# Optimization experiments

Measured on AMD Instinct MI355X. Metric: run time of the kernel, lower is better.

Reference implementation:

```python
import jax, jax.numpy as jnp
import numpy as np

SLOPE = 25.0   # snntorch surrogate.fast_sigmoid default slope
THR = 1.0      # snntorch Leaky default threshold
NUM_STEPS = 100

# fast_sigmoid surrogate spike: heaviside fwd, 1/(slope|x|+1)^2 bwd
@jax.custom_vjp
def spike(x):
    return (x > 0).astype(x.dtype)

def _spike_fwd(x):
    return spike(x), x

def _spike_bwd(x, g):
    return (g / (SLOPE * jnp.abs(x) + 1.0) ** 2,)

spike.defvjp(_spike_fwd, _spike_bwd)


def setup_inputs() -> dict:
    key = jax.random.key(0)
    ks = jax.random.split(key, 5)
    B, D_in, D_h, D_out = 512, 784, 2048, 10
    x = jax.random.normal(ks[0], (B, D_in), dtype=jnp.float32)
    W1 = jax.random.normal(ks[1], (D_h, D_in), dtype=jnp.float32) / np.sqrt(D_in).astype(np.float32)
    b1 = jax.random.normal(ks[2], (D_h,), dtype=jnp.float32) * 0.01
    W2 = jax.random.normal(ks[3], (D_out, D_h), dtype=jnp.float32) / np.sqrt(D_h).astype(np.float32)
    b2 = jax.random.normal(ks[4], (D_out,), dtype=jnp.float32) * 0.01
    beta1 = jnp.asarray(0.9, dtype=jnp.float32)  # learn_beta=True -> parameter
    beta2 = jnp.asarray(0.9, dtype=jnp.float32)
    return {"x": x, "W1": W1, "b1": b1, "W2": W2, "b2": b2, "beta1": beta1, "beta2": beta2}


def reference(x, W1, b1, W2, b2, beta1, beta2):
    dtype = x.dtype
    B = x.shape[0]
    Dh = W1.shape[0]
    Do = W2.shape[0]
    # fc1(x) is loop-invariant in the original (x constant across steps) -> hoist
    cur1 = x @ W1.T + b1                       # [B, Dh]
    b1c = jnp.clip(beta1, 0.0, 1.0)            # snntorch clamps beta in forward
    b2c = jnp.clip(beta2, 0.0, 1.0)
    mem1_0 = jnp.zeros((B, Dh), dtype)         # init_leaky -> 0
    mem2_0 = jnp.zeros((B, Do), dtype)

    def step(carry, _):
        mem1, mem2 = carry
        # snntorch Leaky (reset_mechanism='subtract'):
        # reset_t = detached heaviside(mem_{t-1} - thr); mem_t = beta*mem_{t-1} + cur - reset*thr
        reset1 = jax.lax.stop_gradient((mem1 > THR).astype(dtype))
        mem1 = b1c * mem1 + cur1 - reset1 * THR
        spk1 = spike(mem1 - THR)               # [B, Dh]
        cur2 = spk1 @ W2.T + b2                # [B, Do]
        reset2 = jax.lax.stop_gradient((mem2 > THR).astype(dtype))
        mem2 = b2c * mem2 + cur2 - reset2 * THR
        spk2 = spike(mem2 - THR)
        return (mem1, mem2), spk2

    _, spk2_rec = jax.lax.scan(step, (mem1_0, mem2_0), None, length=NUM_STEPS)  # [T, B, Do]
    # snn_res_step_num == snn_num_steps -> mean over all steps
    stk_mean = jnp.mean(spk2_rec, axis=0)      # [B, Do]
    return jax.nn.softmax(stk_mean, axis=1)
```

## Files before the change

kernel.cpp:

```cpp
#include <hip/hip_runtime.h>
#include <cstdint>

typedef unsigned int u32;
typedef unsigned short u16;
typedef unsigned long long u64;
typedef __attribute__((ext_vector_type(4))) float f32x4;
typedef __attribute__((ext_vector_type(8))) short s16x8;

#define D_IN   784
#define D_H    2048
#define D_O    10
#define T_STEPS 100
#define NCOPY  16

static __device__ __forceinline__ u16 f2bf_rn(float f) {
  u32 u = __float_as_uint(f);
  u32 r = u + 0x7FFFu + ((u >> 16) & 1u);
  return (u16)(r >> 16);
}
static __device__ __forceinline__ float bf2f(u16 h) {
  return __uint_as_float(((u32)h) << 16);
}

static __device__ __forceinline__ void packpair(float f0, float f1,
                                                u32& o0, u32& o1, u32& o2) {
  u32 u0 = __float_as_uint(f0), u1 = __float_as_uint(f1);
  o0 = (u0 >> 16) | (u1 & 0xFFFF0000u);
  float r0 = __fsub_rn(f0, __uint_as_float(u0 & 0xFFFF0000u));
  float r1 = __fsub_rn(f1, __uint_as_float(u1 & 0xFFFF0000u));
  u32 v0 = __float_as_uint(r0), v1 = __float_as_uint(r1);
  o1 = (v0 >> 16) | (v1 & 0xFFFF0000u);
  float s0 = __fsub_rn(r0, __uint_as_float(v0 & 0xFFFF0000u));
  float s1 = __fsub_rn(r1, __uint_as_float(v1 & 0xFFFF0000u));
  o2 = (__float_as_uint(s0) >> 16) | (__float_as_uint(s1) & 0xFFFF0000u);
}

__global__ __launch_bounds__(256) void k_prep_w2(const float* __restrict__ W2,
                                                 u32* __restrict__ Phi,
                                                 u32* __restrict__ Plo) {
  const int blk = blockIdx.x;
  const int copy = blk >> 4;
  int t = (blk & 15) * 256 + threadIdx.x;
  int kb = t >> 6, l = t & 63;
  int o = l & 15;
  int kbase = kb * 32 + ((l >> 4) << 3);
  u32 hw[4], lw[4];
#pragma unroll
  for (int p = 0; p < 4; ++p) {
    u32 hp = 0, lp = 0;
#pragma unroll
    for (int q = 0; q < 2; ++q) {
      float f = (o < D_O) ? W2[o * D_H + kbase + 2 * p + q] : 0.0f;
      u16 h = f2bf_rn(f);
      float rr = __fsub_rn(f, bf2f(h));
      u16 lo = f2bf_rn(rr);
      hp |= ((u32)h) << (16 * q);
      lp |= ((u32)lo) << (16 * q);
    }
    hw[p] = hp; lw[p] = lp;
  }
  int base = (copy << 15) + (kb * 64 + l) * 4;
#pragma unroll
  for (int p = 0; p < 4; ++p) { Phi[base + p] = hw[p]; Plo[base + p] = lw[p]; }
}

__global__ __launch_bounds__(512) void k_fgemm(const float* __restrict__ x,
                                               const float* __restrict__ W1,
                                               const float* __restrict__ b1,
                                               float* __restrict__ cur1) {
  __shared__ uint4 As[2][3][4][64];
  __shared__ uint4 Bs[2][3][4][64];
  const int tid = threadIdx.x, wave = tid >> 6, lane = tid & 63;
  const int id = blockIdx.x;
  const int sub = id >> 3;
  const int mb = sub >> 2;
  const int nb = (id & 7) * 4 + (sub & 3);
  const int wm = wave >> 1, wn = wave & 1;
  const int st = tid & 255;
  const int srow = st >> 2, skq = st & 3;
  const int sfrag = srow >> 4;
  const int slane = skq * 16 + (srow & 15);
  const bool isA = (tid < 256);
  const float* srcrow = isA ? (x  + (size_t)(mb * 64 + srow) * D_IN)
                            : (W1 + (size_t)(nb * 64 + srow) * D_IN);
  f32x4 acc0 = {0.f, 0.f, 0.f, 0.f}, acc1 = {0.f, 0.f, 0.f, 0.f};
  float e[8];
  {
    const int kg = skq * 8;
    float4 v0 = *(const float4*)(srcrow + kg);
    float4 v1 = *(const float4*)(srcrow + kg + 4);
    e[0] = v0.x; e[1] = v0.y; e[2] = v0.z; e[3] = v0.w;
    e[4] = v1.x; e[5] = v1.y; e[6] = v1.z; e[7] = v1.w;
  }
  {
    u32 w0[4], w1[4], w2[4];
#pragma unroll
    for (int p = 0; p < 4; ++p) packpair(e[2 * p], e[2 * p + 1], w0[p], w1[p], w2[p]);
    if (isA) {
      As[0][0][sfrag][slane] = make_uint4(w0[0], w0[1], w0[2], w0[3]);
      As[0][1][sfrag][slane] = make_uint4(w1[0], w1[1], w1[2], w1[3]);
      As[0][2][sfrag][slane] = make_uint4(w2[0], w2[1], w2[2], w2[3]);
    } else {
      Bs[0][0][sfrag][slane] = make_uint4(w0[0], w0[1], w0[2], w0[3]);
      Bs[0][1][sfrag][slane] = make_uint4(w1[0], w1[1], w1[2], w1[3]);
      Bs[0][2][sfrag][slane] = make_uint4(w2[0], w2[1], w2[2], w2[3]);
    }
  }
  __syncthreads();
  for (int kb = 0; kb < 25; ++kb) {
    const int cur = kb & 1, nxt = cur ^ 1;
    if (kb < 24) {
      const int kg = (kb + 1) * 32 + skq * 8;
      if (kg < D_IN) {
        float4 v0 = *(const float4*)(srcrow + kg);
        float4 v1 = *(const float4*)(srcrow + kg + 4);
        e[0] = v0.x; e[1] = v0.y; e[2] = v0.z; e[3] = v0.w;
        e[4] = v1.x; e[5] = v1.y; e[6] = v1.z; e[7] = v1.w;
      } else {
#pragma unroll
        for (int q = 0; q < 8; ++q) e[q] = 0.0f;
      }
    }
    s16x8 A0 = __builtin_bit_cast(s16x8, As[cur][0][wm][lane]);
    s16x8 A1 = __builtin_bit_cast(s16x8, As[cur][1][wm][lane]);
    s16x8 A2 = __builtin_bit_cast(s16x8, As[cur][2][wm][lane]);
    {
      s16x8 B0 = __builtin_bit_cast(s16x8, Bs[cur][0][wn * 2][lane]);
      s16x8 B1 = __builtin_bit_cast(s16x8, Bs[cur][1][wn * 2][lane]);
      s16x8 B2 = __builtin_bit_cast(s16x8, Bs[cur][2][wn * 2][lane]);
      acc0 = __builtin_amdgcn_mfma_f32_16x16x32_bf16(A0, B0, acc0, 0, 0, 0);
      acc0 = __builtin_amdgcn_mfma_f32_16x16x32_bf16(A0, B1, acc0, 0, 0, 0);
      acc0 = __builtin_amdgcn_mfma_f32_16x16x32_bf16(A1, B0, acc0, 0, 0, 0);
      acc0 = __builtin_amdgcn_mfma_f32_16x16x32_bf16(A1, B1, acc0, 0, 0, 0);
      acc0 = __builtin_amdgcn_mfma_f32_16x16x32_bf16(A0, B2, acc0, 0, 0, 0);
      acc0 = __builtin_amdgcn_mfma_f32_16x16x32_bf16(A2, B0, acc0, 0, 0, 0);
    }
    {
      s16x8 B0 = __builtin_bit_cast(s16x8, Bs[cur][0][wn * 2 + 1][lane]);
      s16x8 B1 = __builtin_bit_cast(s16x8, Bs[cur][1][wn * 2 + 1][lane]);
      s16x8 B2 = __builtin_bit_cast(s16x8, Bs[cur][2][wn * 2 + 1][lane]);
      acc1 = __builtin_amdgcn_mfma_f32_16x16x32_bf16(A0, B0, acc1, 0, 0, 0);
      acc1 = __builtin_amdgcn_mfma_f32_16x16x32_bf16(A0, B1, acc1, 0, 0, 0);
      acc1 = __builtin_amdgcn_mfma_f32_16x16x32_bf16(A1, B0, acc1, 0, 0, 0);
      acc1 = __builtin_amdgcn_mfma_f32_16x16x32_bf16(A1, B1, acc1, 0, 0, 0);
      acc1 = __builtin_amdgcn_mfma_f32_16x16x32_bf16(A0, B2, acc1, 0, 0, 0);
      acc1 = __builtin_amdgcn_mfma_f32_16x16x32_bf16(A2, B0, acc1, 0, 0, 0);
    }
    if (kb < 24) {
      u32 w0[4], w1[4], w2[4];
#pragma unroll
      for (int p = 0; p < 4; ++p) packpair(e[2 * p], e[2 * p + 1], w0[p], w1[p], w2[p]);
      if (isA) {
        As[nxt][0][sfrag][slane] = make_uint4(w0[0], w0[1], w0[2], w0[3]);
        As[nxt][1][sfrag][slane] = make_uint4(w1[0], w1[1], w1[2], w1[3]);
        As[nxt][2][sfrag][slane] = make_uint4(w2[0], w2[1], w2[2], w2[3]);
      } else {
        Bs[nxt][0][sfrag][slane] = make_uint4(w0[0], w0[1], w0[2], w0[3]);
        Bs[nxt][1][sfrag][slane] = make_uint4(w1[0], w1[1], w1[2], w1[3]);
        Bs[nxt][2][sfrag][slane] = make_uint4(w2[0], w2[1], w2[2], w2[3]);
      }
    }
    __syncthreads();
  }
  const int col = lane & 15, rb = (lane >> 4) * 4;
  {
    const int gcol = nb * 64 + (wn * 2) * 16 + col;
    const float bv = b1[gcol];
#pragma unroll
    for (int r = 0; r < 4; ++r)
      cur1[(size_t)(mb * 64 + wm * 16 + rb + r) * D_H + gcol] = acc0[r] + bv;
  }
  {
    const int gcol = nb * 64 + (wn * 2 + 1) * 16 + col;
    const float bv = b1[gcol];
#pragma unroll
    for (int r = 0; r < 4; ++r)
      cur1[(size_t)(mb * 64 + wm * 16 + rb + r) * D_H + gcol] = acc1[r] + bv;
  }
}

__global__ __launch_bounds__(512) void k_snn4(const float* __restrict__ cur1,
                                              const u32* __restrict__ Phi,
                                              const u32* __restrict__ Plo,
                                              const float* __restrict__ b2,
                                              const float* __restrict__ beta1p,
                                              const float* __restrict__ beta2p,
                                              float* __restrict__ out) {
  __shared__ __align__(16) u32 bits[112][66];
  __shared__ float c2[112][18];
  const int b = blockIdx.x;
  const int tid = threadIdx.x;
  const int wave = tid >> 6, lane = tid & 63;
  const float b1c = fminf(fmaxf(beta1p[0], 0.0f), 1.0f);
  const float b2c = fminf(fmaxf(beta2p[0], 0.0f), 1.0f);

  for (int idx = tid; idx < 12 * 66; idx += 512) bits[100 + idx / 66][idx % 66] = 0;

  float cv[4], memv[4], spf[4];
#pragma unroll
  for (int j = 0; j < 4; ++j) {
    cv[j] = cur1[(size_t)b * D_H + j * 512 + tid];
    memv[j] = 0.0f; spf[j] = 0.0f;
  }
  for (int t = 0; t < T_STEPS; ++t) {
    u64 msk[4];
#pragma unroll
    for (int j = 0; j < 4; ++j) {
      float m = __fmul_rn(b1c, memv[j]);
      m = __fadd_rn(m, cv[j]);
      m = __fsub_rn(m, spf[j]);
      bool sp = (m > 1.0f);
      msk[j] = __ballot(sp);
      spf[j] = sp ? 1.0f : 0.0f;
      memv[j] = m;
    }
    if (lane == 0) {
      u64* rowp = (u64*)&bits[t][0];
      rowp[0 * 8 + wave] = msk[0];
      rowp[1 * 8 + wave] = msk[1];
      rowp[2 * 8 + wave] = msk[2];
      rowp[3 * 8 + wave] = msk[3];
    }
  }
  __syncthreads();

  if (wave < 7) {
    const u32* PhiB = Phi + ((size_t)(b & (NCOPY - 1)) << 15);
    const u32* PloB = Plo + ((size_t)(b & (NCOPY - 1)) << 15);
    f32x4 acc = {0.f, 0.f, 0.f, 0.f};
    const int row0 = wave * 16 + (lane & 15);
    const int shift = (lane >> 4) * 8;
    for (int kg = 0; kg < 64; kg += 4) {
      uint4 bh[4], bl[4];
#pragma unroll
      for (int i = 0; i < 4; ++i) {
        bh[i] = *(const uint4*)(PhiB + (size_t)(kg + i) * 256 + lane * 4);
        bl[i] = *(const uint4*)(PloB + (size_t)(kg + i) * 256 + lane * 4);
      }
#pragma unroll
      for (int i = 0; i < 4; ++i) {
        u32 w8 = (bits[row0][kg + i] >> shift) & 0xFFu;
        u32 u = w8 | (w8 << 15);
        uint4 a0u;
        ((u32*)&a0u)[0] = ( u        & 0x00010001u) * 0x3F80u;
        ((u32*)&a0u)[1] = ((u >> 2)  & 0x00010001u) * 0x3F80u;
        ((u32*)&a0u)[2] = ((u >> 4)  & 0x00010001u) * 0x3F80u;
        ((u32*)&a0u)[3] = ((u >> 6)  & 0x00010001u) * 0x3F80u;
        s16x8 a   = __builtin_bit_cast(s16x8, a0u);
        s16x8 bhi = __builtin_bit_cast(s16x8, bh[i]);
        s16x8 blo = __builtin_bit_cast(s16x8, bl[i]);
        acc = __builtin_amdgcn_mfma_f32_16x16x32_bf16(a, bhi, acc, 0, 0, 0);
        acc = __builtin_amdgcn_mfma_f32_16x16x32_bf16(a, blo, acc, 0, 0, 0);
      }
    }
    const int colw = lane & 15, rbase = (lane >> 4) * 4;
#pragma unroll
    for (int r = 0; r < 4; ++r) c2[wave * 16 + rbase + r][colw] = acc[r];
  }
  __syncthreads();

  if (tid < 16) {
    const int o = tid;
    const bool valid = (o < D_O);
    const float bb = valid ? b2[o] : 0.0f;
    float m2 = 0.0f; bool s2 = false; int cnt = 0;
    for (int t0 = 0; t0 < T_STEPS; t0 += 10) {
      float cc[10];
#pragma unroll
      for (int i = 0; i < 10; ++i) cc[i] = c2[t0 + i][o];
#pragma unroll
      for (int i = 0; i < 10; ++i) {
        float cI = __fadd_rn(cc[i], bb);
        float m = __fadd_rn(__fmul_rn(b2c, m2), cI);
        if (s2) m = __fsub_rn(m, 1.0f);
        s2 = (m > 1.0f);
        m2 = m;
        cnt += s2 ? 1 : 0;
      }
    }
    float mean = valid ? ((float)cnt / 100.0f) : -1e30f;
    float mx = mean;
#pragma unroll
    for (int i = 8; i >= 1; i >>= 1) mx = fmaxf(mx, __shfl_xor(mx, i, 16));
    float e = valid ? expf(mean - mx) : 0.0f;
    float s = e;
#pragma unroll
    for (int i = 8; i >= 1; i >>= 1) s = __fadd_rn(s, __shfl_xor(s, i, 16));
    if (valid) out[(size_t)b * D_O + o] = e / s;
  }
}

extern "C" void kernel_launch(void* const* d_in, const int* in_sizes, int n_in,
                              void* d_out, int out_size, void* d_ws, size_t ws_size,
                              hipStream_t stream) {
  const float* x     = (const float*)d_in[0];
  const float* W1    = (const float*)d_in[1];
  const float* b1    = (const float*)d_in[2];
  const float* W2    = (const float*)d_in[3];
  const float* b2    = (const float*)d_in[4];
  const float* beta1 = (const float*)d_in[5];
  const float* beta2 = (const float*)d_in[6];
  float* out = (float*)d_out;

  char* ws = (char*)d_ws;
  float* cur1 = (float*)ws;
  u32*   Phi  = (u32*)(ws + 4194304);
  u32*   Plo  = (u32*)(ws + 6291456);

  hipLaunchKernelGGL(k_prep_w2, dim3(256), dim3(256), 0, stream, W2, Phi, Plo);
  hipLaunchKernelGGL(k_fgemm, dim3(256), dim3(512), 0, stream, x, W1, b1, cur1);
  hipLaunchKernelGGL(k_snn4, dim3(512), dim3(512), 0, stream,
                     cur1, Phi, Plo, b2, beta1, beta2, out);
}
```

Baseline: 67.26 us.

## Stage W2 fragments through LDS with async double-buffered loads, drop W2 copies

The spike-by-W2 GEMM in the SNN kernel now streams W2 bf16 hi/lo fragments into shared memory using global_load_lds in a double-buffered loop. All eight waves cooperatively load each chunk while seven waves run MFMAs. This replaces per-wave direct global loads from 16 replicated W2 copies, so the prep kernel shrinks to one copy and 16 blocks. Launch-bounds occupancy hints are also added to the GEMM and SNN kernels. The cost is extra __syncthreads per chunk and about 32KB more LDS per block, which may limit occupancy.

```diff
diff --git a/kernel.cpp b/kernel.cpp
--- a/kernel.cpp
+++ b/kernel.cpp
@@ -11,7 +11,6 @@
 #define D_H    2048
 #define D_O    10
 #define T_STEPS 100
-#define NCOPY  16
 
 static __device__ __forceinline__ u16 f2bf_rn(float f) {
   u32 u = __float_as_uint(f);
@@ -20,6 +19,11 @@
 }
 static __device__ __forceinline__ float bf2f(u16 h) {
   return __uint_as_float(((u32)h) << 16);
+}
+static __device__ __forceinline__ void gl_lds16(const u32* g, void* l) {
+  __builtin_amdgcn_global_load_lds(
+      (const __attribute__((address_space(1))) void*)g,
+      (__attribute__((address_space(3))) void*)l, 16, 0, 0);
 }
 
 static __device__ __forceinline__ void packpair(float f0, float f1,
@@ -38,9 +42,8 @@
 __global__ __launch_bounds__(256) void k_prep_w2(const float* __restrict__ W2,
                                                  u32* __restrict__ Phi,
                                                  u32* __restrict__ Plo) {
-  const int blk = blockIdx.x;
-  const int copy = blk >> 4;
-  int t = (blk & 15) * 256 + threadIdx.x;
+  int t = blockIdx.x * 256 + threadIdx.x;
+  if (t >= 64 * 64) return;
   int kb = t >> 6, l = t & 63;
   int o = l & 15;
   int kbase = kb * 32 + ((l >> 4) << 3);
@@ -59,15 +62,15 @@
     }
     hw[p] = hp; lw[p] = lp;
   }
-  int base = (copy << 15) + (kb * 64 + l) * 4;
+  int base = (kb * 64 + l) * 4;
 #pragma unroll
   for (int p = 0; p < 4; ++p) { Phi[base + p] = hw[p]; Plo[base + p] = lw[p]; }
 }
 
-__global__ __launch_bounds__(512) void k_fgemm(const float* __restrict__ x,
-                                               const float* __restrict__ W1,
-                                               const float* __restrict__ b1,
-                                               float* __restrict__ cur1) {
+__global__ __launch_bounds__(512, 2) void k_fgemm(const float* __restrict__ x,
+                                                  const float* __restrict__ W1,
+                                                  const float* __restrict__ b1,
+                                                  float* __restrict__ cur1) {
   __shared__ uint4 As[2][3][4][64];
   __shared__ uint4 Bs[2][3][4][64];
   const int tid = threadIdx.x, wave = tid >> 6, lane = tid & 63;
@@ -179,15 +182,17 @@
   }
 }
 
-__global__ __launch_bounds__(512) void k_snn4(const float* __restrict__ cur1,
-                                              const u32* __restrict__ Phi,
-                                              const u32* __restrict__ Plo,
-                                              const float* __restrict__ b2,
-                                              const float* __restrict__ beta1p,
-                                              const float* __restrict__ beta2p,
-                                              float* __restrict__ out) {
+__global__ __launch_bounds__(512, 4) void k_snn6(const float* __restrict__ cur1,
+                                                 const u32* __restrict__ Phi,
+                                                 const u32* __restrict__ Plo,
+                                                 const float* __restrict__ b2,
+                                                 const float* __restrict__ beta1p,
+                                                 const float* __restrict__ beta2p,
+                                                 float* __restrict__ out) {
   __shared__ __align__(16) u32 bits[112][66];
   __shared__ float c2[112][18];
+  __shared__ uint4 PhiS[2][8][64];
+  __shared__ uint4 PloS[2][8][64];
   const int b = blockIdx.x;
   const int tid = threadIdx.x;
   const int wave = tid >> 6, lane = tid & 63;
@@ -222,24 +227,29 @@
       rowp[3 * 8 + wave] = msk[3];
     }
   }
+
+  {
+    const size_t r0 = (size_t)(0 * 8 + wave) * 64 + lane;
+    gl_lds16(Phi + r0 * 4, &PhiS[0][wave][0]);
+    gl_lds16(Plo + r0 * 4, &PloS[0][wave][0]);
+  }
   __syncthreads();
 
-  if (wave < 7) {
-    const u32* PhiB = Phi + ((size_t)(b & (NCOPY - 1)) << 15);
-    const u32* PloB = Plo + ((size_t)(b & (NCOPY - 1)) << 15);
-    f32x4 acc = {0.f, 0.f, 0.f, 0.f};
-    const int row0 = wave * 16 + (lane & 15);
-    const int shift = (lane >> 4) * 8;
-    for (int kg = 0; kg < 64; kg += 4) {
-      uint4 bh[4], bl[4];
-#pragma unroll
-      for (int i = 0; i < 4; ++i) {
-        bh[i] = *(const uint4*)(PhiB + (size_t)(kg + i) * 256 + lane * 4);
-        bl[i] = *(const uint4*)(PloB + (size_t)(kg + i) * 256 + lane * 4);
-      }
-#pragma unroll
-      for (int i = 0; i < 4; ++i) {
-        u32 w8 = (bits[row0][kg + i] >> shift) & 0xFFu;
+  f32x4 acc = {0.f, 0.f, 0.f, 0.f};
+  const int row0 = wave * 16 + (lane & 15);
+  const int shift = (lane >> 4) * 8;
+  for (int c = 0; c < 8; ++c) {
+    const int p = c & 1;
+    if (c < 7) {
+      const size_t r0 = (size_t)((c + 1) * 8 + wave) * 64 + lane;
+      gl_lds16(Phi + r0 * 4, &PhiS[p ^ 1][wave][0]);
+      gl_lds16(Plo + r0 * 4, &PloS[p ^ 1][wave][0]);
+    }
+    __builtin_amdgcn_sched_barrier(0);
+    if (wave < 7) {
+#pragma unroll
+      for (int kk = 0; kk < 8; ++kk) {
+        u32 w8 = (bits[row0][c * 8 + kk] >> shift) & 0xFFu;
         u32 u = w8 | (w8 << 15);
         uint4 a0u;
         ((u32*)&a0u)[0] = ( u        & 0x00010001u) * 0x3F80u;
@@ -247,12 +257,15 @@
         ((u32*)&a0u)[2] = ((u >> 4)  & 0x00010001u) * 0x3F80u;
         ((u32*)&a0u)[3] = ((u >> 6)  & 0x00010001u) * 0x3F80u;
         s16x8 a   = __builtin_bit_cast(s16x8, a0u);
-        s16x8 bhi = __builtin_bit_cast(s16x8, bh[i]);
-        s16x8 blo = __builtin_bit_cast(s16x8, bl[i]);
+        s16x8 bhi = __builtin_bit_cast(s16x8, PhiS[p][kk][lane]);
+        s16x8 blo = __builtin_bit_cast(s16x8, PloS[p][kk][lane]);
         acc = __builtin_amdgcn_mfma_f32_16x16x32_bf16(a, bhi, acc, 0, 0, 0);
         acc = __builtin_amdgcn_mfma_f32_16x16x32_bf16(a, blo, acc, 0, 0, 0);
       }
     }
+    __syncthreads();
+  }
+  if (wave < 7) {
     const int colw = lane & 15, rbase = (lane >> 4) * 4;
 #pragma unroll
     for (int r = 0; r < 4; ++r) c2[wave * 16 + rbase + r][colw] = acc[r];
@@ -305,10 +318,10 @@
   char* ws = (char*)d_ws;
   float* cur1 = (float*)ws;
   u32*   Phi  = (u32*)(ws + 4194304);
-  u32*   Plo  = (u32*)(ws + 6291456);
-
-  hipLaunchKernelGGL(k_prep_w2, dim3(256), dim3(256), 0, stream, W2, Phi, Plo);
+  u32*   Plo  = (u32*)(ws + 4259840);
+
+  hipLaunchKernelGGL(k_prep_w2, dim3(16), dim3(256), 0, stream, W2, Phi, Plo);
   hipLaunchKernelGGL(k_fgemm, dim3(256), dim3(512), 0, stream, x, W1, b1, cur1);
-  hipLaunchKernelGGL(k_snn4, dim3(512), dim3(512), 0, stream,
+  hipLaunchKernelGGL(k_snn6, dim3(512), dim3(512), 0, stream,
                      cur1, Phi, Plo, b2, beta1, beta2, out);
 }
```

Measured after the change: 68.33 us. About the same (+1.6%).
